# Performance work log

Hardware: AMD Instinct MI355X
Metric: run time of the kernel (lower is better)

## Reference

```python
import jax, jax.numpy as jnp
import numpy as np

B, T, D, V, L, HM = 4, 2048, 128, 64, 12, 512
EPS = 1e-5
SCALE = float(np.sqrt(D))


def setup_inputs() -> dict:
    key = jax.random.key(0)
    ks = jax.random.split(key, 12)
    s = 0.02
    x = jax.random.randint(ks[0], (B, T), 0, V)
    pos_emb = jax.random.normal(ks[1], (T, D), jnp.float32) * s
    # per-layer params stacked on leading L axis; Linear weights in torch (out,in) layout
    Wq = jax.random.normal(ks[2], (L, D, D), jnp.float32) * s
    Wk = jax.random.normal(ks[3], (L, D, D), jnp.float32) * s
    Wv = jax.random.normal(ks[4], (L, D, D), jnp.float32) * s
    ln1_g = jnp.ones((L, D), jnp.float32)
    ln1_b = jnp.zeros((L, D), jnp.float32)
    W1 = jax.random.normal(ks[5], (L, HM, D), jnp.float32) * s
    b1 = jnp.zeros((L, HM), jnp.float32)
    W2 = jax.random.normal(ks[6], (L, D, HM), jnp.float32) * s
    b2 = jnp.zeros((L, D), jnp.float32)
    ln2_g = jnp.ones((L, D), jnp.float32)
    ln2_b = jnp.zeros((L, D), jnp.float32)
    Wro = jax.random.normal(ks[7], (1, D), jnp.float32) * s
    bro = jnp.zeros((1,), jnp.float32)
    return dict(x=x, pos_emb=pos_emb, Wq=Wq, Wk=Wk, Wv=Wv, ln1_g=ln1_g, ln1_b=ln1_b,
                W1=W1, b1=b1, W2=W2, b2=b2, ln2_g=ln2_g, ln2_b=ln2_b, Wro=Wro, bro=bro)


def _layernorm(h, g, b):
    mu = jnp.mean(h, axis=-1, keepdims=True)
    var = jnp.mean(jnp.square(h - mu), axis=-1, keepdims=True)
    return (h - mu) * jax.lax.rsqrt(var + EPS) * g + b


def _token_embeddings(x):
    # -(c - x)^2 / 2 over class ids, zero-padded up to D
    ar = jnp.arange(V, dtype=jnp.float32)  # [V]
    leave = -jnp.square(ar - x[..., None].astype(jnp.float32)) * 0.5  # [B,T,V]
    return jnp.pad(leave, ((0, 0), (0, 0), (0, D - V)))  # [B,T,D]


def _forward(x, pos_emb, Wq, Wk, Wv, ln1_g, ln1_b, W1, b1, W2, b2, ln2_g, ln2_b, Wro, bro):
    H = _token_embeddings(x) + pos_emb[None]  # [B,T,D]

    def step(Hc, p):
        wq, wk, wv, g1, be1, w1, bb1, w2, bb2, g2, be2 = p
        H1 = _layernorm(Hc, g1, be1)
        q = H1 @ wq.T
        k = H1 @ wk.T
        v = H1 @ wv.T
        scores = jnp.einsum('bid,bjd->bij', q, k) / SCALE  # [B,T,T]
        attn = jax.nn.softmax(scores, axis=-1)
        Hc = Hc + jnp.einsum('bij,bjd->bid', attn, v)
        H2 = _layernorm(Hc, g2, be2)
        Hc = Hc + (jax.nn.gelu(H2 @ w1.T + bb1, approximate=False) @ w2.T + bb2)
        return Hc, None

    H, _ = jax.lax.scan(step, H, (Wq, Wk, Wv, ln1_g, ln1_b, W1, b1, W2, b2, ln2_g, ln2_b))
    pred = H @ Wro.T + bro  # [B,T,1]
    return pred[:, :, 0]


def reference(x, pos_emb, Wq, Wk, Wv, ln1_g, ln1_b, W1, b1, W2, b2, ln2_g, ln2_b, Wro, bro):
    return _forward(x, pos_emb, Wq, Wk, Wv, ln1_g, ln1_b, W1, b1, W2, b2, ln2_g, ln2_b, Wro, bro)
```

## Files before the change

### kernel.cpp

```cpp
#include <hip/hip_runtime.h>
#include <math.h>

#define D 128
#define T 2048
#define BATCH 4
#define HMID 512
#define NLAYER 12

#define KSPLIT 8
#define KPB (T / KSPLIT)
#define BK 64

#if defined(__has_builtin)
#if __has_builtin(__builtin_amdgcn_global_load_lds)
#define USE_GLL 1
#endif
#endif
#ifndef USE_GLL
#define USE_GLL 0
#endif

typedef unsigned short u16;
typedef __attribute__((ext_vector_type(8))) short bf16x8;
typedef __attribute__((ext_vector_type(16))) float f32x16;

__device__ inline u16 f2bf(float x) {
    unsigned u = __builtin_bit_cast(unsigned, x);
    return (u16)((u + 0x7FFFu + ((u >> 16) & 1u)) >> 16);
}
__device__ inline float bf2f(u16 v) {
    return __builtin_bit_cast(float, (unsigned)v << 16);
}
__device__ inline unsigned pkt(float a, float b) {
    return (__builtin_bit_cast(unsigned, a) >> 16) |
           (__builtin_bit_cast(unsigned, b) & 0xFFFF0000u);
}


__device__ inline void ln_stats32(const float (*Ct)[133], float* mu_s, float* rs_s, int tid) {
    const int q = tid >> 3, e8 = tid & 7;
    float s = 0.f;
#pragma unroll
    for (int c = 0; c < 16; c++) s += Ct[q][e8 * 16 + c];
    s += __shfl_xor(s, 1); s += __shfl_xor(s, 2); s += __shfl_xor(s, 4);
    float mu = s * (1.f / D);
    float s2 = 0.f;
#pragma unroll
    for (int c = 0; c < 16; c++) {
        float d0 = Ct[q][e8 * 16 + c] - mu;
        s2 += d0 * d0;
    }
    s2 += __shfl_xor(s2, 1); s2 += __shfl_xor(s2, 2); s2 += __shfl_xor(s2, 4);
    if (e8 == 0) { mu_s[q] = mu; rs_s[q] = rsqrtf(s2 * (1.f / D) + 1e-5f); }
}

__device__ inline void build_as(const float (*Ct)[133], const float* mu_s, const float* rs_s,
                                const float* __restrict__ g, const float* __restrict__ bb,
                                u16* As, int tid) {
    const int row = tid >> 3, e8 = tid & 7;
    const float mu = mu_s[row], rs = rs_s[row];
#pragma unroll
    for (int cc = 0; cc < 2; cc++) {
        int c = e8 * 2 + cc;
        u16 tmp[8];
#pragma unroll
        for (int j = 0; j < 8; j++) {
            int d = c * 8 + j;
            tmp[j] = f2bf((Ct[row][d] - mu) * rs * g[d] + bb[d]);
        }
        *(uint4*)&As[((size_t)c * 32 + (row ^ (c & 7))) * 8] = *(uint4*)tmp;
    }
}

__device__ inline void stage_w(const u16* __restrict__ W, int ldw, u16* Wst, int tid) {
#pragma unroll
    for (int i = 0; i < 8; i++) {
        int ci = tid + 256 * i;
        int row = ci >> 4, c = ci & 15;
        *(uint4*)&Wst[((size_t)c * 128 + (row ^ c)) * 8] =
            *(const uint4*)(W + (size_t)row * ldw + c * 8);
    }
}

__device__ inline f32x16 mm_32x128(const u16* As, const u16* Wst, int wv, int ql, int h) {
    f32x16 a;
#pragma unroll
    for (int r = 0; r < 16; r++) a[r] = 0.f;
#pragma unroll
    for (int s = 0; s < 8; s++) {
        int ch = 2 * s + h;
        bf16x8 af = *(const bf16x8*)&As[((size_t)ch * 32 + (ql ^ (ch & 7))) * 8];
        bf16x8 bf = *(const bf16x8*)&Wst[((size_t)ch * 128 + ((wv * 32 + ql) ^ ch)) * 8];
        a = __builtin_amdgcn_mfma_f32_32x32x16_bf16(af, bf, a, 0, 0, 0);
    }
    return a;
}

__device__ inline void qkv_phase(const u16* As, const u16* __restrict__ Wqkvl, u16* Wst,
                                 u16* __restrict__ qb, u16* __restrict__ kb,
                                 u16* __restrict__ vt, int m0, int tid) {
    const int wv = tid >> 6, l = tid & 63, h = l >> 5, ql = l & 31;
    const int bbk = m0 >> 11;
    const int tl0 = m0 & 2047;
#pragma unroll
    for (int sl = 0; sl < 3; sl++) {
        __syncthreads();
        stage_w(Wqkvl + (size_t)sl * 128 * D, D, Wst, tid);
        __syncthreads();
        f32x16 a = mm_32x128(As, Wst, wv, ql, h);
        const int n = wv * 32 + ql;
        if (sl == 2) {
            u16* dst = vt + (size_t)bbk * D * T + (size_t)n * T + tl0;
#pragma unroll
            for (int g = 0; g < 4; g++) {
                ushort4 o;
                o.x = f2bf(a[4 * g + 0]);
                o.y = f2bf(a[4 * g + 1]);
                o.z = f2bf(a[4 * g + 2]);
                o.w = f2bf(a[4 * g + 3]);
                *(ushort4*)(dst + 8 * g + 4 * h) = o;
            }
        } else {
            u16* dst = (sl == 0) ? qb : kb;
#pragma unroll
            for (int r = 0; r < 16; r++) {
                int row = (r & 3) + 8 * (r >> 2) + 4 * h;
                dst[(size_t)(m0 + row) * D + n] = f2bf(a[r]);
            }
        }
    }
}

__global__ __launch_bounds__(256) void conv_all(const float* __restrict__ Wq,
                                                const float* __restrict__ Wk,
                                                const float* __restrict__ Wv,
                                                const float* __restrict__ W1,
                                                const float* __restrict__ W2,
                                                u16* __restrict__ Wqkv,
                                                u16* __restrict__ W1b,
                                                u16* __restrict__ W2b, float qscale) {
    const int NQ = NLAYER * 3 * D * D;
    const int NW = NLAYER * HMID * D;
    int idx = blockIdx.x * 256 + threadIdx.x;
    if (idx < NQ) {
        int lN = idx / (3 * D * D);
        int rem = idx - lN * (3 * D * D);
        int s = rem >> 14;
        int off = rem & 16383;
        const float* src = (s == 0) ? Wq : ((s == 1) ? Wk : Wv);
        Wqkv[idx] = f2bf(src[lN * 16384 + off] * ((s == 0) ? qscale : 1.f));
    } else if (idx < NQ + NW) {
        W1b[idx - NQ] = f2bf(W1[idx - NQ]);
    } else if (idx < NQ + 2 * NW) {
        W2b[idx - NQ - NW] = f2bf(W2[idx - NQ - NW]);
    }
}

__global__ __launch_bounds__(256, 1) void embed_qkv(const int* __restrict__ x,
                                                    const float* __restrict__ pos,
                                                    const float* __restrict__ g1,
                                                    const float* __restrict__ b1g,
                                                    const u16* __restrict__ Wqkv0,
                                                    u16* __restrict__ qb, u16* __restrict__ kb,
                                                    u16* __restrict__ vt,
                                                    float* __restrict__ H) {
    __shared__ float Ct[32][133];
    __shared__ float mu_s[32], rs_s[32];
    __shared__ u16 As[16 * 32 * 8];
    __shared__ u16 Wst[16 * 128 * 8];
    const int tid = threadIdx.x;
    const int m0 = blockIdx.x * 32;
    {
        const int d = tid & 127, rr = tid >> 7;
#pragma unroll
        for (int i = 0; i < 16; i++) {
            int row = rr * 16 + i;
            int tok = m0 + row;
            int t = tok & (T - 1);
            float e = 0.f;
            if (d < 64) {
                float diff = (float)d - (float)x[tok];
                e = -0.5f * diff * diff;
            }
            float v = e + pos[(size_t)t * D + d];
            Ct[row][d] = v;
            H[(size_t)tok * D + d] = v;
        }
    }
    __syncthreads();
    ln_stats32(Ct, mu_s, rs_s, tid);
    __syncthreads();
    build_as(Ct, mu_s, rs_s, g1, b1g, As, tid);
    qkv_phase(As, Wqkv0, Wst, qb, kb, vt, m0, tid);
}

__global__ __launch_bounds__(256, 2) void attn_mfma(const u16* __restrict__ qg,
                                                    const u16* __restrict__ kg,
                                                    const u16* __restrict__ vtg,
                                                    u16* __restrict__ Op,
                                                    float* __restrict__ ml) {
    __shared__ u16 Ks[64 * 128];
    __shared__ u16 Vt[128 * 64];
    const int tid = threadIdx.x;
    const int w = tid >> 6;
    const int l = tid & 63;
    const int h = l >> 5;
    const int ql = l & 31;
    const int qblk = blockIdx.x;
    const int ks = blockIdx.y;
    const int b = qblk >> 4;

    const size_t qrow = (size_t)qblk * 128 + w * 32 + ql;
    bf16x8 qf[8];
#pragma unroll
    for (int c = 0; c < 8; c++)
        qf[c] = *(const bf16x8*)(qg + qrow * D + c * 16 + h * 8);

    f32x16 ot[4];
#pragma unroll
    for (int t = 0; t < 4; t++)
#pragma unroll
        for (int r = 0; r < 16; r++) ot[t][r] = 0.f;
    float m_run = -1e30f, l_run = 0.f;

    const size_t kgb = (size_t)b * T * D;
    const size_t vtb = (size_t)b * D * T;

    for (int kt = 0; kt < KPB / BK; kt++) {
        const int kbase = ks * KPB + kt * BK;
        __syncthreads();
#if USE_GLL
#pragma unroll
        for (int i = 0; i < 4; i++) {
            int s = w * 256 + i * 64 + l;
            int row = s >> 4, ch = (s & 15) ^ (row & 7);
            __builtin_amdgcn_global_load_lds(
                (const __attribute__((address_space(1))) void*)(kg + kgb + (size_t)(kbase + row) * D + ch * 8),
                (__attribute__((address_space(3))) void*)&Ks[(w * 256 + i * 64) * 8], 16, 0, 0);
        }
#pragma unroll
        for (int i = 0; i < 4; i++) {
            int s = w * 256 + i * 64 + l;
            int dd = s >> 3, ch = (s & 7) ^ (dd & 7);
            __builtin_amdgcn_global_load_lds(
                (const __attribute__((address_space(1))) void*)(vtg + vtb + (size_t)dd * T + kbase + ch * 8),
                (__attribute__((address_space(3))) void*)&Vt[(w * 256 + i * 64) * 8], 16, 0, 0);
        }
#else
#pragma unroll
        for (int i = 0; i < 4; i++) {
            int s = tid + i * 256;
            int row = s >> 4, ch = (s & 15) ^ (row & 7);
            *(uint4*)&Ks[(size_t)s * 8] = *(const uint4*)(kg + kgb + (size_t)(kbase + row) * D + ch * 8);
            int dd = s >> 3, ch2 = (s & 7) ^ (dd & 7);
            *(uint4*)&Vt[(size_t)s * 8] = *(const uint4*)(vtg + vtb + (size_t)dd * T + kbase + ch2 * 8);
        }
#endif
        __syncthreads();
        f32x16 st0, st1;
#pragma unroll
        for (int r = 0; r < 16; r++) { st0[r] = 0.f; st1[r] = 0.f; }
#pragma unroll
        for (int c = 0; c < 8; c++) {
            int ch = c * 2 + h;
            bf16x8 k0 = *(const bf16x8*)&Ks[(ql * 16 + (ch ^ (ql & 7))) * 8];
            bf16x8 k1 = *(const bf16x8*)&Ks[((32 + ql) * 16 + (ch ^ (ql & 7))) * 8];
            st0 = __builtin_amdgcn_mfma_f32_32x32x16_bf16(k0, qf[c], st0, 0, 0, 0);
            st1 = __builtin_amdgcn_mfma_f32_32x32x16_bf16(k1, qf[c], st1, 0, 0, 0);
        }
        float mx = m_run;
#pragma unroll
        for (int r = 0; r < 16; r++) mx = fmaxf(mx, fmaxf(st0[r], st1[r]));
        mx = fmaxf(mx, __shfl_xor(mx, 32));
        float alpha = exp2f(m_run - mx);
        m_run = mx;
        float rs = 0.f;
#pragma unroll
        for (int r = 0; r < 16; r++) {
            float p0 = exp2f(st0[r] - mx); st0[r] = p0;
            float p1 = exp2f(st1[r] - mx); st1[r] = p1;
            rs += p0 + p1;
        }
        rs += __shfl_xor(rs, 32);
        l_run = l_run * alpha + rs;
        uint2 pk0[4], pk1[4];
#pragma unroll
        for (int g = 0; g < 4; g++) {
            pk0[g].x = pkt(st0[4 * g + 0], st0[4 * g + 1]);
            pk0[g].y = pkt(st0[4 * g + 2], st0[4 * g + 3]);
            pk1[g].x = pkt(st1[4 * g + 0], st1[4 * g + 1]);
            pk1[g].y = pkt(st1[4 * g + 2], st1[4 * g + 3]);
        }
#pragma unroll
        for (int t = 0; t < 4; t++)
#pragma unroll
            for (int r = 0; r < 16; r++) ot[t][r] *= alpha;
#pragma unroll
        for (int c = 0; c < 4; c++) {
            const uint2* pk = (c < 2) ? pk0 : pk1;
            const int cc = c & 1;
            uint2 own = h ? pk[2 * cc + 1] : pk[2 * cc];
            uint2 snd = h ? pk[2 * cc] : pk[2 * cc + 1];
            uint2 rcv;
            rcv.x = (unsigned)__shfl_xor((int)snd.x, 32);
            rcv.y = (unsigned)__shfl_xor((int)snd.y, 32);
            uint4 fr;
            fr.x = h ? rcv.x : own.x;
            fr.y = h ? rcv.y : own.y;
            fr.z = h ? own.x : rcv.x;
            fr.w = h ? own.y : rcv.y;
            bf16x8 pf = __builtin_bit_cast(bf16x8, fr);
            int ch = c * 2 + h;
#pragma unroll
            for (int t = 0; t < 4; t++) {
                bf16x8 vf = *(const bf16x8*)&Vt[((t * 32 + ql) * 8 + (ch ^ (ql & 7))) * 8];
                ot[t] = __builtin_amdgcn_mfma_f32_32x32x16_bf16(vf, pf, ot[t], 0, 0, 0);
            }
        }
    }
    size_t base = (((size_t)(qblk * KSPLIT + ks)) * 4 + w) * (128 * 32);
#pragma unroll
    for (int t = 0; t < 4; t++)
#pragma unroll
        for (int r = 0; r < 16; r++) {
            int dd = (r & 3) + 8 * (r >> 2) + 4 * h + 32 * t;
            Op[base + (size_t)dd * 32 + ql] = f2bf(ot[t][r]);
        }
    if (h == 0) {
        int qi = w * 32 + ql;
        ml[(size_t)(qblk * KSPLIT + ks) * 256 + qi] = m_run;
        ml[(size_t)(qblk * KSPLIT + ks) * 256 + 128 + qi] = l_run;
    }
}

template <int LAST>
__global__ __launch_bounds__(256, 1) void layer_tail(
    const u16* __restrict__ Op, const float* __restrict__ ml,
    float* __restrict__ H,
    const float* __restrict__ g2, const float* __restrict__ b2l,
    const u16* __restrict__ W1l, const float* __restrict__ b1l,
    const u16* __restrict__ W2l, const float* __restrict__ b2bias,
    const float* __restrict__ g1n, const float* __restrict__ b1n,
    const u16* __restrict__ Wqkvn,
    u16* __restrict__ qb, u16* __restrict__ kb, u16* __restrict__ vt,
    const float* __restrict__ Wro, const float* __restrict__ bro,
    float* __restrict__ outp) {
    __shared__ float Ct[32][133];
    __shared__ float mu_s[32], rs_s[32];
    __shared__ u16 As[16 * 32 * 8];
    __shared__ u16 midS[64 * 32 * 8];
    __shared__ u16 Wst[16 * 128 * 8];

    const int tid = threadIdx.x;
    const int bid = blockIdx.x;
    const int qblk = bid >> 2;
    const int wq = bid & 3;
    const int m0 = bid * 32;
    const int wv = tid >> 6;
    const int l = tid & 63;
    const int h = l >> 5;
    const int ql = l & 31;

    {
        const int dg = tid >> 5;
        float m[KSPLIT], lv[KSPLIT];
        float M = -1e30f;
#pragma unroll
        for (int ks = 0; ks < KSPLIT; ks++) {
            m[ks] = ml[(size_t)(qblk * KSPLIT + ks) * 256 + wq * 32 + ql];
            lv[ks] = ml[(size_t)(qblk * KSPLIT + ks) * 256 + 128 + wq * 32 + ql];
            M = fmaxf(M, m[ks]);
        }
        float L = 0.f, f[KSPLIT];
#pragma unroll
        for (int ks = 0; ks < KSPLIT; ks++) { f[ks] = exp2f(m[ks] - M); L += lv[ks] * f[ks]; }
        float invL = 1.f / L;
        float acc[16];
#pragma unroll
        for (int i = 0; i < 16; i++) acc[i] = 0.f;
#pragma unroll
        for (int ks = 0; ks < KSPLIT; ks++) {
            size_t base = (((size_t)(qblk * KSPLIT + ks)) * 4 + wq) * (128 * 32);
#pragma unroll
            for (int i = 0; i < 16; i++)
                acc[i] += bf2f(Op[base + (size_t)(dg * 16 + i) * 32 + ql]) * f[ks];
        }
#pragma unroll
        for (int i = 0; i < 16; i++) Ct[ql][dg * 16 + i] = acc[i] * invL;
    }
    __syncthreads();
    {
        const int d = tid & 127, rr = tid >> 7;
#pragma unroll
        for (int i = 0; i < 16; i++) {
            int row = rr * 16 + i;
            Ct[row][d] += H[(size_t)(m0 + row) * D + d];
        }
    }
    __syncthreads();
    ln_stats32(Ct, mu_s, rs_s, tid);
    __syncthreads();
    build_as(Ct, mu_s, rs_s, g2, b2l, As, tid);
#pragma unroll
    for (int nc = 0; nc < 4; nc++) {
        __syncthreads();
        stage_w(W1l + (size_t)nc * 128 * D, D, Wst, tid);
        __syncthreads();
        f32x16 a = mm_32x128(As, Wst, wv, ql, h);
        const int n = nc * 128 + wv * 32 + ql;
        const int ch2 = n >> 3, sub = n & 7;
        const float bv = b1l[n];
#pragma unroll
        for (int r = 0; r < 16; r++) {
            int row = (r & 3) + 8 * (r >> 2) + 4 * h;
            float v = a[r] + bv;
            v = 0.5f * v * (1.f + erff(v * 0.7071067811865475f));
            midS[((size_t)ch2 * 32 + (row ^ (ch2 & 7))) * 8 + sub] = f2bf(v);
        }
    }
    f32x16 a2;
#pragma unroll
    for (int r = 0; r < 16; r++) a2[r] = 0.f;
#pragma unroll
    for (int kc = 0; kc < 4; kc++) {
        __syncthreads();
        stage_w(W2l + (size_t)kc * 128, HMID, Wst, tid);
        __syncthreads();
#pragma unroll
        for (int s = 0; s < 8; s++) {
            int ch = 2 * s + h;
            int gch = kc * 16 + ch;
            bf16x8 af = *(const bf16x8*)&midS[((size_t)gch * 32 + (ql ^ (gch & 7))) * 8];
            bf16x8 bf = *(const bf16x8*)&Wst[((size_t)ch * 128 + ((wv * 32 + ql) ^ ch)) * 8];
            a2 = __builtin_amdgcn_mfma_f32_32x32x16_bf16(af, bf, a2, 0, 0, 0);
        }
    }
    {
        const int col = wv * 32 + ql;
        const float bv = b2bias[col];
#pragma unroll
        for (int r = 0; r < 16; r++) {
            int row = (r & 3) + 8 * (r >> 2) + 4 * h;
            float v = a2[r] + bv + Ct[row][col];
            Ct[row][col] = v;
            H[(size_t)(m0 + row) * D + col] = v;
        }
    }
    __syncthreads();
    if (LAST) {
        const int q = tid >> 3, e8 = tid & 7;
        float s = 0.f;
#pragma unroll
        for (int c = 0; c < 16; c++) s += Ct[q][e8 * 16 + c] * Wro[e8 * 16 + c];
        s += __shfl_xor(s, 1); s += __shfl_xor(s, 2); s += __shfl_xor(s, 4);
        if (e8 == 0) outp[m0 + q] = s + bro[0];
    } else {
        ln_stats32(Ct, mu_s, rs_s, tid);
        __syncthreads();
        build_as(Ct, mu_s, rs_s, g1n, b1n, As, tid);
        qkv_phase(As, Wqkvn, Wst, qb, kb, vt, m0, tid);
    }
}

extern "C" void kernel_launch(void* const* d_in, const int* in_sizes, int n_in,
                              void* d_out, int out_size, void* d_ws, size_t ws_size,
                              hipStream_t stream) {
    const int* x = (const int*)d_in[0];
    const float* pos = (const float*)d_in[1];
    const float* Wq = (const float*)d_in[2];
    const float* Wk = (const float*)d_in[3];
    const float* Wv = (const float*)d_in[4];
    const float* ln1g = (const float*)d_in[5];
    const float* ln1b = (const float*)d_in[6];
    const float* W1 = (const float*)d_in[7];
    const float* b1 = (const float*)d_in[8];
    const float* W2 = (const float*)d_in[9];
    const float* b2 = (const float*)d_in[10];
    const float* ln2g = (const float*)d_in[11];
    const float* ln2b = (const float*)d_in[12];
    const float* Wro = (const float*)d_in[13];
    const float* bro = (const float*)d_in[14];
    float* out = (float*)d_out;

    const size_t NTOK = (size_t)BATCH * T;
    const size_t HSZ = NTOK * D;
    float* ws = (float*)d_ws;
    float* H = ws;
    u16* qb = (u16*)(ws + HSZ);
    u16* kb = (u16*)(ws + HSZ + HSZ / 2);
    u16* vt = (u16*)(ws + 2 * HSZ);
    u16* Op = (u16*)(ws + 2 * HSZ + HSZ / 2);
    float* mlbuf = ws + 7 * HSZ;
    u16* Wqkv = (u16*)(ws + 7 * HSZ + 131072);
    u16* W1b = Wqkv + (size_t)NLAYER * 3 * D * D;
    u16* W2b = W1b + (size_t)NLAYER * HMID * D;

    const float qscale = 1.4426950408889634f / 11.313708498984761f;

    conv_all<<<dim3(8448), 256, 0, stream>>>(Wq, Wk, Wv, W1, W2, Wqkv, W1b, W2b, qscale);
    embed_qkv<<<dim3(256), 256, 0, stream>>>(x, pos, ln1g, ln1b, Wqkv, qb, kb, vt, H);

    for (int lay = 0; lay < NLAYER; lay++) {
        attn_mfma<<<dim3(64, KSPLIT), 256, 0, stream>>>(qb, kb, vt, Op, mlbuf);
        if (lay < NLAYER - 1) {
            layer_tail<0><<<dim3(256), 256, 0, stream>>>(
                Op, mlbuf, H,
                ln2g + (size_t)lay * D, ln2b + (size_t)lay * D,
                W1b + (size_t)lay * HMID * D, b1 + (size_t)lay * HMID,
                W2b + (size_t)lay * D * HMID, b2 + (size_t)lay * D,
                ln1g + (size_t)(lay + 1) * D, ln1b + (size_t)(lay + 1) * D,
                Wqkv + (size_t)(lay + 1) * 3 * D * D,
                qb, kb, vt, Wro, bro, nullptr);
        } else {
            layer_tail<1><<<dim3(256), 256, 0, stream>>>(
                Op, mlbuf, H,
                ln2g + (size_t)lay * D, ln2b + (size_t)lay * D,
                W1b + (size_t)lay * HMID * D, b1 + (size_t)lay * HMID,
                W2b + (size_t)lay * D * HMID, b2 + (size_t)lay * D,
                ln1g, ln1b, Wqkv,
                qb, kb, vt, Wro, bro, out);
        }
    }
}
```

Before: 633.4 us.

## Fuse whole forward into persistent megakernel with grid barriers

```diff
diff --git a/kernel.cpp b/kernel.cpp
--- a/kernel.cpp
+++ b/kernel.cpp
@@ -6,10 +6,7 @@
 #define BATCH 4
 #define HMID 512
 #define NLAYER 12
-
-#define KSPLIT 8
-#define KPB (T / KSPLIT)
-#define BK 64
+#define NBLK 256
 
 #if defined(__has_builtin)
 #if __has_builtin(__builtin_amdgcn_global_load_lds)
@@ -36,29 +33,55 @@
            (__builtin_bit_cast(unsigned, b) & 0xFFFF0000u);
 }
 
-
-__device__ inline void ln_stats32(const float (*Ct)[133], float* mu_s, float* rs_s, int tid) {
+struct SM {
+    float Hl[32][133];
+    u16 Qs[16][32][8];
+    float mstat[4][2][32];
+    float Lbuf[32];
+    float mu_s[32], rs_s[32];
+    union {
+        u16 KV[4][16384];
+        struct {
+            u16 As[16][32][8];
+            u16 midS[64][32][8];
+            u16 Wst[16][128][8];
+        } tl;
+    } u;
+};
+
+__device__ inline void grid_barrier(unsigned* slot) {
+    __syncthreads();
+    if (threadIdx.x == 0) {
+        __threadfence();
+        atomicAdd(slot, 1u);
+        while (__hip_atomic_load(slot, __ATOMIC_ACQUIRE, __HIP_MEMORY_SCOPE_AGENT) < (unsigned)NBLK)
+            __builtin_amdgcn_s_sleep(8);
+        __threadfence();
+    }
+    __syncthreads();
+}
+
+__device__ inline void ln_stats32(SM& sm, int tid) {
     const int q = tid >> 3, e8 = tid & 7;
     float s = 0.f;
 #pragma unroll
-    for (int c = 0; c < 16; c++) s += Ct[q][e8 * 16 + c];
+    for (int c = 0; c < 16; c++) s += sm.Hl[q][e8 * 16 + c];
     s += __shfl_xor(s, 1); s += __shfl_xor(s, 2); s += __shfl_xor(s, 4);
     float mu = s * (1.f / D);
     float s2 = 0.f;
 #pragma unroll
     for (int c = 0; c < 16; c++) {
-        float d0 = Ct[q][e8 * 16 + c] - mu;
+        float d0 = sm.Hl[q][e8 * 16 + c] - mu;
         s2 += d0 * d0;
     }
     s2 += __shfl_xor(s2, 1); s2 += __shfl_xor(s2, 2); s2 += __shfl_xor(s2, 4);
-    if (e8 == 0) { mu_s[q] = mu; rs_s[q] = rsqrtf(s2 * (1.f / D) + 1e-5f); }
-}
-
-__device__ inline void build_as(const float (*Ct)[133], const float* mu_s, const float* rs_s,
-                                const float* __restrict__ g, const float* __restrict__ bb,
-                                u16* As, int tid) {
+    if (e8 == 0) { sm.mu_s[q] = mu; sm.rs_s[q] = rsqrtf(s2 * (1.f / D) + 1e-5f); }
+}
+
+__device__ inline void build_as(SM& sm, const float* __restrict__ g,
+                                const float* __restrict__ bb, int tid) {
     const int row = tid >> 3, e8 = tid & 7;
-    const float mu = mu_s[row], rs = rs_s[row];
+    const float mu = sm.mu_s[row], rs = sm.rs_s[row];
 #pragma unroll
     for (int cc = 0; cc < 2; cc++) {
         int c = e8 * 2 + cc;
@@ -66,156 +89,99 @@
 #pragma unroll
         for (int j = 0; j < 8; j++) {
             int d = c * 8 + j;
-            tmp[j] = f2bf((Ct[row][d] - mu) * rs * g[d] + bb[d]);
-        }
-        *(uint4*)&As[((size_t)c * 32 + (row ^ (c & 7))) * 8] = *(uint4*)tmp;
-    }
-}
-
-__device__ inline void stage_w(const u16* __restrict__ W, int ldw, u16* Wst, int tid) {
+            tmp[j] = f2bf((sm.Hl[row][d] - mu) * rs * g[d] + bb[d]);
+        }
+        *(uint4*)&sm.u.tl.As[c][row ^ (c & 7)][0] = *(uint4*)tmp;
+    }
+}
+
+__device__ inline void stage_w(const u16* __restrict__ W, int ldw, SM& sm, int tid) {
 #pragma unroll
     for (int i = 0; i < 8; i++) {
         int ci = tid + 256 * i;
         int row = ci >> 4, c = ci & 15;
-        *(uint4*)&Wst[((size_t)c * 128 + (row ^ c)) * 8] =
-            *(const uint4*)(W + (size_t)row * ldw + c * 8);
-    }
-}
-
-__device__ inline f32x16 mm_32x128(const u16* As, const u16* Wst, int wv, int ql, int h) {
+        *(uint4*)&sm.u.tl.Wst[c][row ^ c][0] = *(const uint4*)(W + (size_t)row * ldw + c * 8);
+    }
+}
+
+__device__ inline f32x16 mm_32x128(SM& sm, int wv, int ql, int h) {
     f32x16 a;
 #pragma unroll
     for (int r = 0; r < 16; r++) a[r] = 0.f;
 #pragma unroll
     for (int s = 0; s < 8; s++) {
         int ch = 2 * s + h;
-        bf16x8 af = *(const bf16x8*)&As[((size_t)ch * 32 + (ql ^ (ch & 7))) * 8];
-        bf16x8 bf = *(const bf16x8*)&Wst[((size_t)ch * 128 + ((wv * 32 + ql) ^ ch)) * 8];
+        bf16x8 af = *(const bf16x8*)&sm.u.tl.As[ch][ql ^ (ch & 7)][0];
+        bf16x8 bf = *(const bf16x8*)&sm.u.tl.Wst[ch][(wv * 32 + ql) ^ ch][0];
         a = __builtin_amdgcn_mfma_f32_32x32x16_bf16(af, bf, a, 0, 0, 0);
     }
     return a;
 }
 
-__device__ inline void qkv_phase(const u16* As, const u16* __restrict__ Wqkvl, u16* Wst,
-                                 u16* __restrict__ qb, u16* __restrict__ kb,
-                                 u16* __restrict__ vt, int m0, int tid) {
+__device__ inline void qkv_phase(SM& sm, const u16* __restrict__ Wqkvl,
+                                 u16* __restrict__ kbn, u16* __restrict__ vtn,
+                                 int m0, int bq, int tid) {
     const int wv = tid >> 6, l = tid & 63, h = l >> 5, ql = l & 31;
-    const int bbk = m0 >> 11;
-    const int tl0 = m0 & 2047;
-#pragma unroll
-    for (int sl = 0; sl < 3; sl++) {
-        __syncthreads();
-        stage_w(Wqkvl + (size_t)sl * 128 * D, D, Wst, tid);
-        __syncthreads();
-        f32x16 a = mm_32x128(As, Wst, wv, ql, h);
+    const int tl0 = m0 & (T - 1);
+    __syncthreads();
+    stage_w(Wqkvl, D, sm, tid);
+    __syncthreads();
+    {
+        f32x16 aq;
+#pragma unroll
+        for (int r = 0; r < 16; r++) aq[r] = 0.f;
+#pragma unroll
+        for (int s = 0; s < 8; s++) {
+            int ch = 2 * s + h;
+            bf16x8 af = *(const bf16x8*)&sm.u.tl.As[ch][ql ^ (ch & 7)][0];
+            bf16x8 bf = *(const bf16x8*)&sm.u.tl.Wst[ch][(wv * 32 + ql) ^ ch][0];
+            aq = __builtin_amdgcn_mfma_f32_32x32x16_bf16(bf, af, aq, 0, 0, 0);
+        }
+#pragma unroll
+        for (int g = 0; g < 4; g++) {
+            ushort4 o;
+            o.x = f2bf(aq[4 * g + 0]); o.y = f2bf(aq[4 * g + 1]);
+            o.z = f2bf(aq[4 * g + 2]); o.w = f2bf(aq[4 * g + 3]);
+            *(ushort4*)&sm.Qs[4 * wv + g][ql][4 * h] = o;
+        }
+    }
+    __syncthreads();
+    stage_w(Wqkvl + 128 * D, D, sm, tid);
+    __syncthreads();
+    {
+        f32x16 a = mm_32x128(sm, wv, ql, h);
         const int n = wv * 32 + ql;
-        if (sl == 2) {
-            u16* dst = vt + (size_t)bbk * D * T + (size_t)n * T + tl0;
-#pragma unroll
-            for (int g = 0; g < 4; g++) {
-                ushort4 o;
-                o.x = f2bf(a[4 * g + 0]);
-                o.y = f2bf(a[4 * g + 1]);
-                o.z = f2bf(a[4 * g + 2]);
-                o.w = f2bf(a[4 * g + 3]);
-                *(ushort4*)(dst + 8 * g + 4 * h) = o;
-            }
-        } else {
-            u16* dst = (sl == 0) ? qb : kb;
-#pragma unroll
-            for (int r = 0; r < 16; r++) {
-                int row = (r & 3) + 8 * (r >> 2) + 4 * h;
-                dst[(size_t)(m0 + row) * D + n] = f2bf(a[r]);
-            }
-        }
-    }
-}
-
-__global__ __launch_bounds__(256) void conv_all(const float* __restrict__ Wq,
-                                                const float* __restrict__ Wk,
-                                                const float* __restrict__ Wv,
-                                                const float* __restrict__ W1,
-                                                const float* __restrict__ W2,
-                                                u16* __restrict__ Wqkv,
-                                                u16* __restrict__ W1b,
-                                                u16* __restrict__ W2b, float qscale) {
-    const int NQ = NLAYER * 3 * D * D;
-    const int NW = NLAYER * HMID * D;
-    int idx = blockIdx.x * 256 + threadIdx.x;
-    if (idx < NQ) {
-        int lN = idx / (3 * D * D);
-        int rem = idx - lN * (3 * D * D);
-        int s = rem >> 14;
-        int off = rem & 16383;
-        const float* src = (s == 0) ? Wq : ((s == 1) ? Wk : Wv);
-        Wqkv[idx] = f2bf(src[lN * 16384 + off] * ((s == 0) ? qscale : 1.f));
-    } else if (idx < NQ + NW) {
-        W1b[idx - NQ] = f2bf(W1[idx - NQ]);
-    } else if (idx < NQ + 2 * NW) {
-        W2b[idx - NQ - NW] = f2bf(W2[idx - NQ - NW]);
-    }
-}
-
-__global__ __launch_bounds__(256, 1) void embed_qkv(const int* __restrict__ x,
-                                                    const float* __restrict__ pos,
-                                                    const float* __restrict__ g1,
-                                                    const float* __restrict__ b1g,
-                                                    const u16* __restrict__ Wqkv0,
-                                                    u16* __restrict__ qb, u16* __restrict__ kb,
-                                                    u16* __restrict__ vt,
-                                                    float* __restrict__ H) {
-    __shared__ float Ct[32][133];
-    __shared__ float mu_s[32], rs_s[32];
-    __shared__ u16 As[16 * 32 * 8];
-    __shared__ u16 Wst[16 * 128 * 8];
-    const int tid = threadIdx.x;
-    const int m0 = blockIdx.x * 32;
-    {
-        const int d = tid & 127, rr = tid >> 7;
-#pragma unroll
-        for (int i = 0; i < 16; i++) {
-            int row = rr * 16 + i;
-            int tok = m0 + row;
-            int t = tok & (T - 1);
-            float e = 0.f;
-            if (d < 64) {
-                float diff = (float)d - (float)x[tok];
-                e = -0.5f * diff * diff;
-            }
-            float v = e + pos[(size_t)t * D + d];
-            Ct[row][d] = v;
-            H[(size_t)tok * D + d] = v;
-        }
-    }
-    __syncthreads();
-    ln_stats32(Ct, mu_s, rs_s, tid);
-    __syncthreads();
-    build_as(Ct, mu_s, rs_s, g1, b1g, As, tid);
-    qkv_phase(As, Wqkv0, Wst, qb, kb, vt, m0, tid);
-}
-
-__global__ __launch_bounds__(256, 2) void attn_mfma(const u16* __restrict__ qg,
-                                                    const u16* __restrict__ kg,
-                                                    const u16* __restrict__ vtg,
-                                                    u16* __restrict__ Op,
-                                                    float* __restrict__ ml) {
-    __shared__ u16 Ks[64 * 128];
-    __shared__ u16 Vt[128 * 64];
-    const int tid = threadIdx.x;
-    const int w = tid >> 6;
-    const int l = tid & 63;
-    const int h = l >> 5;
-    const int ql = l & 31;
-    const int qblk = blockIdx.x;
-    const int ks = blockIdx.y;
-    const int b = qblk >> 4;
-
-    const size_t qrow = (size_t)qblk * 128 + w * 32 + ql;
+#pragma unroll
+        for (int r = 0; r < 16; r++) {
+            int row = (r & 3) + 8 * (r >> 2) + 4 * h;
+            kbn[(size_t)(m0 + row) * D + n] = f2bf(a[r]);
+        }
+    }
+    __syncthreads();
+    stage_w(Wqkvl + 2 * 128 * D, D, sm, tid);
+    __syncthreads();
+    {
+        f32x16 a = mm_32x128(sm, wv, ql, h);
+        const int n = wv * 32 + ql;
+        u16* dst = vtn + (size_t)bq * D * T + (size_t)n * T + tl0;
+#pragma unroll
+        for (int g = 0; g < 4; g++) {
+            ushort4 o;
+            o.x = f2bf(a[4 * g + 0]); o.y = f2bf(a[4 * g + 1]);
+            o.z = f2bf(a[4 * g + 2]); o.w = f2bf(a[4 * g + 3]);
+            *(ushort4*)(dst + 8 * g + 4 * h) = o;
+        }
+    }
+}
+
+__device__ inline void attn_phase(SM& sm, const u16* __restrict__ kbl,
+                                  const u16* __restrict__ vtl, int tid) {
+    const int w = tid >> 6, l = tid & 63, h = l >> 5, ql = l & 31;
+    u16* Kw = &sm.u.KV[w][0];
+    u16* Vw = &sm.u.KV[w][8192];
     bf16x8 qf[8];
 #pragma unroll
-    for (int c = 0; c < 8; c++)
-        qf[c] = *(const bf16x8*)(qg + qrow * D + c * 16 + h * 8);
-
+    for (int c = 0; c < 8; c++) qf[c] = *(const bf16x8*)&sm.Qs[2 * c + h][ql][0];
     f32x16 ot[4];
 #pragma unroll
     for (int t = 0; t < 4; t++)
@@ -223,50 +189,47 @@
         for (int r = 0; r < 16; r++) ot[t][r] = 0.f;
     float m_run = -1e30f, l_run = 0.f;
 
-    const size_t kgb = (size_t)b * T * D;
-    const size_t vtb = (size_t)b * D * T;
-
-    for (int kt = 0; kt < KPB / BK; kt++) {
-        const int kbase = ks * KPB + kt * BK;
-        __syncthreads();
+    for (int kt = 0; kt < 8; kt++) {
+        const int k0 = w * 512 + kt * 64;
 #if USE_GLL
-#pragma unroll
-        for (int i = 0; i < 4; i++) {
-            int s = w * 256 + i * 64 + l;
+        __builtin_amdgcn_s_waitcnt(0xC07F);
+#pragma unroll
+        for (int i = 0; i < 16; i++) {
+            int s = i * 64 + l;
             int row = s >> 4, ch = (s & 15) ^ (row & 7);
             __builtin_amdgcn_global_load_lds(
-                (const __attribute__((address_space(1))) void*)(kg + kgb + (size_t)(kbase + row) * D + ch * 8),
-                (__attribute__((address_space(3))) void*)&Ks[(w * 256 + i * 64) * 8], 16, 0, 0);
-        }
-#pragma unroll
-        for (int i = 0; i < 4; i++) {
-            int s = w * 256 + i * 64 + l;
+                (const __attribute__((address_space(1))) void*)(kbl + (size_t)(k0 + row) * D + ch * 8),
+                (__attribute__((address_space(3))) void*)(Kw + i * 512), 16, 0, 0);
+        }
+#pragma unroll
+        for (int i = 0; i < 16; i++) {
+            int s = i * 64 + l;
             int dd = s >> 3, ch = (s & 7) ^ (dd & 7);
             __builtin_amdgcn_global_load_lds(
-                (const __attribute__((address_space(1))) void*)(vtg + vtb + (size_t)dd * T + kbase + ch * 8),
-                (__attribute__((address_space(3))) void*)&Vt[(w * 256 + i * 64) * 8], 16, 0, 0);
-        }
+                (const __attribute__((address_space(1))) void*)(vtl + (size_t)dd * T + k0 + ch * 8),
+                (__attribute__((address_space(3))) void*)(Vw + i * 512), 16, 0, 0);
+        }
+        __builtin_amdgcn_s_waitcnt(0x0F70);
 #else
 #pragma unroll
-        for (int i = 0; i < 4; i++) {
-            int s = tid + i * 256;
+        for (int i = 0; i < 16; i++) {
+            int s = i * 64 + l;
             int row = s >> 4, ch = (s & 15) ^ (row & 7);
-            *(uint4*)&Ks[(size_t)s * 8] = *(const uint4*)(kg + kgb + (size_t)(kbase + row) * D + ch * 8);
+            *(uint4*)(Kw + (size_t)s * 8) = *(const uint4*)(kbl + (size_t)(k0 + row) * D + ch * 8);
             int dd = s >> 3, ch2 = (s & 7) ^ (dd & 7);
-            *(uint4*)&Vt[(size_t)s * 8] = *(const uint4*)(vtg + vtb + (size_t)dd * T + kbase + ch2 * 8);
+            *(uint4*)(Vw + (size_t)s * 8) = *(const uint4*)(vtl + (size_t)dd * T + k0 + ch2 * 8);
         }
 #endif
-        __syncthreads();
         f32x16 st0, st1;
 #pragma unroll
         for (int r = 0; r < 16; r++) { st0[r] = 0.f; st1[r] = 0.f; }
 #pragma unroll
         for (int c = 0; c < 8; c++) {
             int ch = c * 2 + h;
-            bf16x8 k0 = *(const bf16x8*)&Ks[(ql * 16 + (ch ^ (ql & 7))) * 8];
-            bf16x8 k1 = *(const bf16x8*)&Ks[((32 + ql) * 16 + (ch ^ (ql & 7))) * 8];
-            st0 = __builtin_amdgcn_mfma_f32_32x32x16_bf16(k0, qf[c], st0, 0, 0, 0);
-            st1 = __builtin_amdgcn_mfma_f32_32x32x16_bf16(k1, qf[c], st1, 0, 0, 0);
+            bf16x8 k0f = *(const bf16x8*)&Kw[((size_t)ql * 16 + (ch ^ (ql & 7))) * 8];
+            bf16x8 k1f = *(const bf16x8*)&Kw[((size_t)(32 + ql) * 16 + (ch ^ (ql & 7))) * 8];
+            st0 = __builtin_amdgcn_mfma_f32_32x32x16_bf16(k0f, qf[c], st0, 0, 0, 0);
+            st1 = __builtin_amdgcn_mfma_f32_32x32x16_bf16(k1f, qf[c], st1, 0, 0, 0);
         }
         float mx = m_run;
 #pragma unroll
@@ -313,100 +276,57 @@
             int ch = c * 2 + h;
 #pragma unroll
             for (int t = 0; t < 4; t++) {
-                bf16x8 vf = *(const bf16x8*)&Vt[((t * 32 + ql) * 8 + (ch ^ (ql & 7))) * 8];
+                bf16x8 vf = *(const bf16x8*)&Vw[(((size_t)(t * 32 + ql)) * 8 + (ch ^ (ql & 7))) * 8];
                 ot[t] = __builtin_amdgcn_mfma_f32_32x32x16_bf16(vf, pf, ot[t], 0, 0, 0);
             }
         }
     }
-    size_t base = (((size_t)(qblk * KSPLIT + ks)) * 4 + w) * (128 * 32);
+    if (h == 0) { sm.mstat[w][0][ql] = m_run; sm.mstat[w][1][ql] = l_run; }
+    __syncthreads();
+    float M = fmaxf(fmaxf(sm.mstat[0][0][ql], sm.mstat[1][0][ql]),
+                    fmaxf(sm.mstat[2][0][ql], sm.mstat[3][0][ql]));
+    float L = 0.f;
+#pragma unroll
+    for (int ww = 0; ww < 4; ww++) L += sm.mstat[ww][1][ql] * exp2f(sm.mstat[ww][0][ql] - M);
+    float fown = exp2f(m_run - M);
+    float* Ow = (float*)&sm.u.KV[w][0];
 #pragma unroll
     for (int t = 0; t < 4; t++)
 #pragma unroll
         for (int r = 0; r < 16; r++) {
             int dd = (r & 3) + 8 * (r >> 2) + 4 * h + 32 * t;
-            Op[base + (size_t)dd * 32 + ql] = f2bf(ot[t][r]);
-        }
-    if (h == 0) {
-        int qi = w * 32 + ql;
-        ml[(size_t)(qblk * KSPLIT + ks) * 256 + qi] = m_run;
-        ml[(size_t)(qblk * KSPLIT + ks) * 256 + 128 + qi] = l_run;
-    }
-}
-
-template <int LAST>
-__global__ __launch_bounds__(256, 1) void layer_tail(
-    const u16* __restrict__ Op, const float* __restrict__ ml,
-    float* __restrict__ H,
-    const float* __restrict__ g2, const float* __restrict__ b2l,
-    const u16* __restrict__ W1l, const float* __restrict__ b1l,
-    const u16* __restrict__ W2l, const float* __restrict__ b2bias,
-    const float* __restrict__ g1n, const float* __restrict__ b1n,
-    const u16* __restrict__ Wqkvn,
-    u16* __restrict__ qb, u16* __restrict__ kb, u16* __restrict__ vt,
-    const float* __restrict__ Wro, const float* __restrict__ bro,
-    float* __restrict__ outp) {
-    __shared__ float Ct[32][133];
-    __shared__ float mu_s[32], rs_s[32];
-    __shared__ u16 As[16 * 32 * 8];
-    __shared__ u16 midS[64 * 32 * 8];
-    __shared__ u16 Wst[16 * 128 * 8];
-
-    const int tid = threadIdx.x;
-    const int bid = blockIdx.x;
-    const int qblk = bid >> 2;
-    const int wq = bid & 3;
-    const int m0 = bid * 32;
-    const int wv = tid >> 6;
-    const int l = tid & 63;
-    const int h = l >> 5;
-    const int ql = l & 31;
-
-    {
-        const int dg = tid >> 5;
-        float m[KSPLIT], lv[KSPLIT];
-        float M = -1e30f;
-#pragma unroll
-        for (int ks = 0; ks < KSPLIT; ks++) {
-            m[ks] = ml[(size_t)(qblk * KSPLIT + ks) * 256 + wq * 32 + ql];
-            lv[ks] = ml[(size_t)(qblk * KSPLIT + ks) * 256 + 128 + wq * 32 + ql];
-            M = fmaxf(M, m[ks]);
-        }
-        float L = 0.f, f[KSPLIT];
-#pragma unroll
-        for (int ks = 0; ks < KSPLIT; ks++) { f[ks] = exp2f(m[ks] - M); L += lv[ks] * f[ks]; }
-        float invL = 1.f / L;
-        float acc[16];
-#pragma unroll
-        for (int i = 0; i < 16; i++) acc[i] = 0.f;
-#pragma unroll
-        for (int ks = 0; ks < KSPLIT; ks++) {
-            size_t base = (((size_t)(qblk * KSPLIT + ks)) * 4 + wq) * (128 * 32);
-#pragma unroll
-            for (int i = 0; i < 16; i++)
-                acc[i] += bf2f(Op[base + (size_t)(dg * 16 + i) * 32 + ql]) * f[ks];
-        }
-#pragma unroll
-        for (int i = 0; i < 16; i++) Ct[ql][dg * 16 + i] = acc[i] * invL;
-    }
-    __syncthreads();
-    {
-        const int d = tid & 127, rr = tid >> 7;
-#pragma unroll
-        for (int i = 0; i < 16; i++) {
-            int row = rr * 16 + i;
-            Ct[row][d] += H[(size_t)(m0 + row) * D + d];
-        }
-    }
-    __syncthreads();
-    ln_stats32(Ct, mu_s, rs_s, tid);
-    __syncthreads();
-    build_as(Ct, mu_s, rs_s, g2, b2l, As, tid);
+            Ow[dd * 32 + ql] = ot[t][r] * fown;
+        }
+    if (w == 0 && h == 0) sm.Lbuf[ql] = 1.f / L;
+    __syncthreads();
+    const int q2 = tid & 31, dg8 = tid >> 5;
+    float invL = sm.Lbuf[q2];
+#pragma unroll
+    for (int i = 0; i < 16; i++) {
+        int d = dg8 * 16 + i;
+        float s = 0.f;
+#pragma unroll
+        for (int ww = 0; ww < 4; ww++) s += ((const float*)&sm.u.KV[ww][0])[d * 32 + q2];
+        sm.Hl[q2][d] += s * invL;
+    }
+    __syncthreads();
+}
+
+__device__ inline void tail_phase(SM& sm, const float* __restrict__ g2,
+                                  const float* __restrict__ b2l,
+                                  const u16* __restrict__ W1l, const float* __restrict__ b1l,
+                                  const u16* __restrict__ W2l, const float* __restrict__ b2bias,
+                                  int tid) {
+    const int wv = tid >> 6, l = tid & 63, h = l >> 5, ql = l & 31;
+    ln_stats32(sm, tid);
+    __syncthreads();
+    build_as(sm, g2, b2l, tid);
 #pragma unroll
     for (int nc = 0; nc < 4; nc++) {
         __syncthreads();
-        stage_w(W1l + (size_t)nc * 128 * D, D, Wst, tid);
+        stage_w(W1l + (size_t)nc * 128 * D, D, sm, tid);
         __syncthreads();
-        f32x16 a = mm_32x128(As, Wst, wv, ql, h);
+        f32x16 a = mm_32x128(sm, wv, ql, h);
         const int n = nc * 128 + wv * 32 + ql;
         const int ch2 = n >> 3, sub = n & 7;
         const float bv = b1l[n];
@@ -415,7 +335,7 @@
             int row = (r & 3) + 8 * (r >> 2) + 4 * h;
             float v = a[r] + bv;
             v = 0.5f * v * (1.f + erff(v * 0.7071067811865475f));
-            midS[((size_t)ch2 * 32 + (row ^ (ch2 & 7))) * 8 + sub] = f2bf(v);
+            sm.u.tl.midS[ch2][row ^ (ch2 & 7)][sub] = f2bf(v);
         }
     }
     f32x16 a2;
@@ -424,14 +344,14 @@
 #pragma unroll
     for (int kc = 0; kc < 4; kc++) {
         __syncthreads();
-        stage_w(W2l + (size_t)kc * 128, HMID, Wst, tid);
+        stage_w(W2l + (size_t)kc * 128, HMID, sm, tid);
         __syncthreads();
 #pragma unroll
         for (int s = 0; s < 8; s++) {
             int ch = 2 * s + h;
             int gch = kc * 16 + ch;
-            bf16x8 af = *(const bf16x8*)&midS[((size_t)gch * 32 + (ql ^ (gch & 7))) * 8];
-            bf16x8 bf = *(const bf16x8*)&Wst[((size_t)ch * 128 + ((wv * 32 + ql) ^ ch)) * 8];
+            bf16x8 af = *(const bf16x8*)&sm.u.tl.midS[gch][ql ^ (gch & 7)][0];
+            bf16x8 bf = *(const bf16x8*)&sm.u.tl.Wst[ch][(wv * 32 + ql) ^ ch][0];
             a2 = __builtin_amdgcn_mfma_f32_32x32x16_bf16(af, bf, a2, 0, 0, 0);
         }
     }
@@ -441,24 +361,95 @@
 #pragma unroll
         for (int r = 0; r < 16; r++) {
             int row = (r & 3) + 8 * (r >> 2) + 4 * h;
-            float v = a2[r] + bv + Ct[row][col];
-            Ct[row][col] = v;
-            H[(size_t)(m0 + row) * D + col] = v;
-        }
-    }
-    __syncthreads();
-    if (LAST) {
-        const int q = tid >> 3, e8 = tid & 7;
-        float s = 0.f;
-#pragma unroll
-        for (int c = 0; c < 16; c++) s += Ct[q][e8 * 16 + c] * Wro[e8 * 16 + c];
-        s += __shfl_xor(s, 1); s += __shfl_xor(s, 2); s += __shfl_xor(s, 4);
-        if (e8 == 0) outp[m0 + q] = s + bro[0];
-    } else {
-        ln_stats32(Ct, mu_s, rs_s, tid);
-        __syncthreads();
-        build_as(Ct, mu_s, rs_s, g1n, b1n, As, tid);
-        qkv_phase(As, Wqkvn, Wst, qb, kb, vt, m0, tid);
+            sm.Hl[row][col] += a2[r] + bv;
+        }
+    }
+    __syncthreads();
+}
+
+__global__ __launch_bounds__(256, 1) void megakernel(
+    const int* __restrict__ x, const float* __restrict__ pos,
+    const float* __restrict__ Wq, const float* __restrict__ Wk, const float* __restrict__ Wv,
+    const float* __restrict__ ln1g, const float* __restrict__ ln1b,
+    const float* __restrict__ W1, const float* __restrict__ b1,
+    const float* __restrict__ W2, const float* __restrict__ b2,
+    const float* __restrict__ ln2g, const float* __restrict__ ln2b,
+    const float* __restrict__ Wro, const float* __restrict__ bro,
+    float* __restrict__ out,
+    u16* __restrict__ Wqkv, u16* __restrict__ W1b, u16* __restrict__ W2b,
+    u16* __restrict__ kb0, u16* __restrict__ vt0,
+    u16* __restrict__ kb1, u16* __restrict__ vt1,
+    unsigned* __restrict__ bar) {
+    __shared__ SM sm;
+    const int tid = threadIdx.x;
+    const int bid = blockIdx.x;
+    const int m0 = bid * 32;
+    const int bq = bid >> 6;
+    int bslot = 0;
+    const float QSCALE = 1.4426950408889634f / 11.313708498984761f;
+
+    {
+        const int NQ = NLAYER * 3 * D * D, NW = NLAYER * HMID * D;
+        for (int idx = bid * 256 + tid; idx < NQ + 2 * NW; idx += NBLK * 256) {
+            if (idx < NQ) {
+                int lN = idx / (3 * D * D);
+                int rem = idx - lN * (3 * D * D);
+                int s = rem >> 14, off = rem & 16383;
+                const float* src = (s == 0) ? Wq : ((s == 1) ? Wk : Wv);
+                Wqkv[idx] = f2bf(src[lN * 16384 + off] * ((s == 0) ? QSCALE : 1.f));
+            } else if (idx < NQ + NW) {
+                W1b[idx - NQ] = f2bf(W1[idx - NQ]);
+            } else {
+                W2b[idx - NQ - NW] = f2bf(W2[idx - NQ - NW]);
+            }
+        }
+    }
+    grid_barrier(&bar[bslot++]);
+
+    {
+        const int d = tid & 127, rr = tid >> 7;
+#pragma unroll
+        for (int i = 0; i < 16; i++) {
+            int row = rr * 16 + i;
+            int tok = m0 + row;
+            float e = 0.f;
+            if (d < 64) {
+                float df = (float)d - (float)x[tok];
+                e = -0.5f * df * df;
+            }
+            sm.Hl[row][d] = e + pos[(size_t)(tok & (T - 1)) * D + d];
+        }
+    }
+    __syncthreads();
+    ln_stats32(sm, tid);
+    __syncthreads();
+    build_as(sm, ln1g, ln1b, tid);
+    qkv_phase(sm, Wqkv, kb0, vt0, m0, bq, tid);
+    grid_barrier(&bar[bslot++]);
+
+    for (int lay = 0; lay < NLAYER; lay++) {
+        const u16* kbr = (lay & 1) ? kb1 : kb0;
+        const u16* vtr = (lay & 1) ? vt1 : vt0;
+        attn_phase(sm, kbr + (size_t)bq * T * D, vtr + (size_t)bq * D * T, tid);
+        tail_phase(sm, ln2g + (size_t)lay * D, ln2b + (size_t)lay * D,
+                   W1b + (size_t)lay * HMID * D, b1 + (size_t)lay * HMID,
+                   W2b + (size_t)lay * D * HMID, b2 + (size_t)lay * D, tid);
+        if (lay < NLAYER - 1) {
+            ln_stats32(sm, tid);
+            __syncthreads();
+            build_as(sm, ln1g + (size_t)(lay + 1) * D, ln1b + (size_t)(lay + 1) * D, tid);
+            u16* kbn = ((lay + 1) & 1) ? kb1 : kb0;
+            u16* vtn = ((lay + 1) & 1) ? vt1 : vt0;
+            qkv_phase(sm, Wqkv + (size_t)(lay + 1) * 3 * D * D, kbn, vtn, m0, bq, tid);
+            grid_barrier(&bar[bslot++]);
+        } else {
+            const int q = tid >> 3, e8 = tid & 7;
+            float s = 0.f;
+#pragma unroll
+            for (int c = 0; c < 16; c++) s += sm.Hl[q][e8 * 16 + c] * Wro[e8 * 16 + c];
+            s += __shfl_xor(s, 1); s += __shfl_xor(s, 2); s += __shfl_xor(s, 4);
+            if (e8 == 0) out[m0 + q] = s + bro[0];
+        }
     }
 }
 
@@ -482,43 +473,18 @@
     const float* bro = (const float*)d_in[14];
     float* out = (float*)d_out;
 
-    const size_t NTOK = (size_t)BATCH * T;
-    const size_t HSZ = NTOK * D;
-    float* ws = (float*)d_ws;
-    float* H = ws;
-    u16* qb = (u16*)(ws + HSZ);
-    u16* kb = (u16*)(ws + HSZ + HSZ / 2);
-    u16* vt = (u16*)(ws + 2 * HSZ);
-    u16* Op = (u16*)(ws + 2 * HSZ + HSZ / 2);
-    float* mlbuf = ws + 7 * HSZ;
-    u16* Wqkv = (u16*)(ws + 7 * HSZ + 131072);
+    u16* wsu = (u16*)d_ws;
+    u16* kb0 = wsu;
+    u16* vt0 = wsu + 1048576;
+    u16* kb1 = wsu + 2097152;
+    u16* vt1 = wsu + 3145728;
+    u16* Wqkv = wsu + 4194304;
     u16* W1b = Wqkv + (size_t)NLAYER * 3 * D * D;
     u16* W2b = W1b + (size_t)NLAYER * HMID * D;
-
-    const float qscale = 1.4426950408889634f / 11.313708498984761f;
-
-    conv_all<<<dim3(8448), 256, 0, stream>>>(Wq, Wk, Wv, W1, W2, Wqkv, W1b, W2b, qscale);
-    embed_qkv<<<dim3(256), 256, 0, stream>>>(x, pos, ln1g, ln1b, Wqkv, qb, kb, vt, H);
-
-    for (int lay = 0; lay < NLAYER; lay++) {
-        attn_mfma<<<dim3(64, KSPLIT), 256, 0, stream>>>(qb, kb, vt, Op, mlbuf);
-        if (lay < NLAYER - 1) {
-            layer_tail<0><<<dim3(256), 256, 0, stream>>>(
-                Op, mlbuf, H,
-                ln2g + (size_t)lay * D, ln2b + (size_t)lay * D,
-                W1b + (size_t)lay * HMID * D, b1 + (size_t)lay * HMID,
-                W2b + (size_t)lay * D * HMID, b2 + (size_t)lay * D,
-                ln1g + (size_t)(lay + 1) * D, ln1b + (size_t)(lay + 1) * D,
-                Wqkv + (size_t)(lay + 1) * 3 * D * D,
-                qb, kb, vt, Wro, bro, nullptr);
-        } else {
-            layer_tail<1><<<dim3(256), 256, 0, stream>>>(
-                Op, mlbuf, H,
-                ln2g + (size_t)lay * D, ln2b + (size_t)lay * D,
-                W1b + (size_t)lay * HMID * D, b1 + (size_t)lay * HMID,
-                W2b + (size_t)lay * D * HMID, b2 + (size_t)lay * D,
-                ln1g, ln1b, Wqkv,
-                qb, kb, vt, Wro, bro, out);
-        }
-    }
-}
+    unsigned* bar = (unsigned*)((char*)d_ws + 14 * 1024 * 1024);
+
+    hipMemsetAsync(bar, 0, 16 * sizeof(unsigned), stream);
+    megakernel<<<dim3(NBLK), dim3(256), 0, stream>>>(
+        x, pos, Wq, Wk, Wv, ln1g, ln1b, W1, b1, W2, b2, ln2g, ln2b, Wro, bro, out,
+        Wqkv, W1b, W2b, kb0, vt0, kb1, vt1, bar);
+}
```

Measured after the change: 1.385 ms. 119% more time.
